# Performance work log

Measured on AMD Instinct MI355X. Metric: run time of the kernel, lower is better.

The kernel has to match this reference:

```python
import jax, jax.numpy as jnp
import numpy as np

B, TQ, M, D, H, F, L = 4, 512, 512, 1024, 16, 4096, 6
S = D // H
R = TQ + M  # relative-attention length = memory + query
CUTOFFS = [20000, 40000, 200000]
PROJ_FACTOR = 4
LN_EPS = 1e-6
NEG_INF = -1e9


def setup_inputs() -> dict:
    key = jax.random.key(0)
    ks = iter(jax.random.split(key, 64))

    def w(shape, scale=0.02):
        return jax.random.normal(next(ks), shape, jnp.float32) * scale

    inp = {}
    inp['token_ids'] = jax.random.randint(next(ks), (B, TQ), 0, CUTOFFS[-1])
    inp['memories'] = w((L, B, M, D))
    starts = [0] + CUTOFFS
    pf = 1
    for i in range(len(CUTOFFS)):
        psize = max(1, D // pf)
        inp['emb_table%d' % i] = w((starts[i + 1] - starts[i], psize))
        inp['emb_proj%d' % i] = w((psize, D))
        pf *= PROJ_FACTOR
    inp['wq'] = w((L, D, H, S)); inp['wk'] = w((L, D, H, S))
    inp['wv'] = w((L, D, H, S)); inp['wr'] = w((L, D, H, S))
    inp['wo'] = w((L, H, S, D))
    inp['content_bias'] = w((L, H, S)); inp['position_bias'] = w((L, H, S))
    inp['ln1_scale'] = jnp.ones((L, D)); inp['ln1_bias'] = jnp.zeros((L, D))
    inp['ln2_scale'] = jnp.ones((L, D)); inp['ln2_bias'] = jnp.zeros((L, D))
    inp['ffn_w1'] = w((L, D, F)); inp['ffn_b1'] = jnp.zeros((L, F))
    inp['ffn_w2'] = w((L, F, D)); inp['ffn_b2'] = jnp.zeros((L, D))
    return inp


def layernorm(x, scale, bias):
    mu = jnp.mean(x, axis=-1, keepdims=True)
    var = jnp.var(x, axis=-1, keepdims=True)
    return (x - mu) * jax.lax.rsqrt(var + LN_EPS) * scale + bias


def rel_shift(x):
    # x: [B, H, Q, R] -> shifted so position j aligns with relative distance
    b, h, q, r = x.shape
    x = jnp.pad(x, ((0, 0), (0, 0), (0, 0), (1, 0)))
    x = x.reshape(b, h, r + 1, q)[:, :, 1:, :]
    return x.reshape(b, h, q, r)


def positional_encoding(r_len, d):
    pos = jnp.arange(r_len - 1, -1, -1, dtype=jnp.float32)  # r_len-1 ... 0
    inv_freq = 1.0 / (10000.0 ** (jnp.arange(0, d, 2, dtype=jnp.float32) / d))
    sinusoid = pos[:, None] * inv_freq[None, :]
    return jnp.concatenate([jnp.sin(sinusoid), jnp.cos(sinusoid)], axis=-1)


def adaptive_embed(ids, tables, projs):
    # jit-friendly version of AdaptiveEmbedding.compute_embeddings:
    # gather per-cluster, project up to D, combine via masks.
    d = projs[0].shape[-1]
    y = jnp.zeros(ids.shape + (d,), jnp.float32)
    starts = [0] + CUTOFFS
    for tab, proj, lo, hi in zip(tables, projs, starts[:-1], starts[1:]):
        mask = (ids >= lo) & (ids < hi)
        idx = jnp.clip(ids - lo, 0, tab.shape[0] - 1)
        emb = jnp.einsum('btp,pd->btd', tab[idx], proj)
        y = y + jnp.where(mask[..., None], emb, 0.0)
    return y * (d ** 0.5)


def transformer_xl(token_ids, memories, emb_tables, emb_projs, wq, wk, wv, wr,
                   wo, content_bias, position_bias, ln1_scale, ln1_bias,
                   ln2_scale, ln2_bias, ffn_w1, ffn_b1, ffn_w2, ffn_b2):
    x = adaptive_embed(token_ids, emb_tables, emb_projs)  # [B, TQ, D]
    pe = positional_encoding(R, D)                        # [R, D]
    q_idx = jnp.arange(TQ)[:, None]
    r_idx = jnp.arange(R)[None, :]
    future = r_idx > q_idx + M                            # [TQ, R], True=masked
    scale = 1.0 / np.sqrt(S).astype(np.float32)
    for l in range(L):
        q = jnp.einsum('btd,dhs->bths', x, wq[l])
        kv_in = jnp.concatenate([memories[l], x], axis=1)  # [B, R, D]
        k = jnp.einsum('brd,dhs->brhs', kv_in, wk[l])
        v = jnp.einsum('brd,dhs->brhs', kv_in, wv[l])
        r = jnp.einsum('rd,dhs->rhs', pe, wr[l])
        ac = jnp.einsum('bqhs,brhs->bhqr', q + content_bias[l], k)
        bd = rel_shift(jnp.einsum('bqhs,rhs->bhqr', q + position_bias[l], r))
        scores = (ac + bd) * scale
        scores = jnp.where(future[None, None], NEG_INF, scores)
        attn = jax.nn.softmax(scores, axis=-1)
        ctx = jnp.einsum('bhqr,brhs->bqhs', attn, v)
        out = jnp.einsum('bqhs,hsd->bqd', ctx, wo[l])
        x = layernorm(x + out, ln1_scale[l], ln1_bias[l])
        h = jax.nn.relu(jnp.einsum('btd,df->btf', x, ffn_w1[l]) + ffn_b1[l])
        h = jnp.einsum('btf,fd->btd', h, ffn_w2[l]) + ffn_b2[l]
        x = layernorm(x + h, ln2_scale[l], ln2_bias[l])
    return x


def reference(token_ids, memories, emb_table0, emb_proj0, emb_table1,
              emb_proj1, emb_table2, emb_proj2, wq, wk, wv, wr, wo,
              content_bias, position_bias, ln1_scale, ln1_bias, ln2_scale,
              ln2_bias, ffn_w1, ffn_b1, ffn_w2, ffn_b2):
    return transformer_xl(
        token_ids, memories,
        [emb_table0, emb_table1, emb_table2],
        [emb_proj0, emb_proj1, emb_proj2],
        wq, wk, wv, wr, wo, content_bias, position_bias,
        ln1_scale, ln1_bias, ln2_scale, ln2_bias,
        ffn_w1, ffn_b1, ffn_w2, ffn_b2)
```

## Files before the change

kernel.cpp:

```cpp
#include <hip/hip_runtime.h>


#define Bc 4
#define TQc 512
#define Mc 512
#define Dc 1024
#define Hc 16
#define Sc 64
#define Fc 4096
#define Lc 6
#define Rc 1024
#define KCAT 1344
#define DDc ((size_t)Dc * Dc)
#define NEG_INF_F (-1e9f)

typedef unsigned short ushortT;
typedef __attribute__((ext_vector_type(8))) short bfrag;
typedef __attribute__((ext_vector_type(4))) float facc;

__device__ inline ushortT f2bf(float f) {
    unsigned int u = __builtin_bit_cast(unsigned int, f);
    u = (u + 0x7FFFu + ((u >> 16) & 1u)) >> 16;
    return (ushortT)u;
}

#define CP16(gp, lp)                                                        \
    __builtin_amdgcn_global_load_lds(                                       \
        (const __attribute__((address_space(1))) unsigned int*)(gp),        \
        (__attribute__((address_space(3))) unsigned int*)(lp), 16, 0, 0)

__device__ inline bfrag lds_frag(const ushortT* lds, int row, int cg) {
    int c = cg ^ (row & 7);
    return *reinterpret_cast<const bfrag*>(
        reinterpret_cast<const char*>(lds) + row * 128 + c * 16);
}

template<int BM, int BN, int OUTM, bool BIAS, bool RELU, bool DUALQ,
         bool KVSRC = false, bool KVOUT = false>
__global__ __launch_bounds__(256) void mgemm(
    const ushortT* __restrict__ A, const ushortT* __restrict__ A2,
    const ushortT* __restrict__ Bt,
    const float* __restrict__ bias, const float* __restrict__ bias2,
    float* __restrict__ Cf, ushortT* __restrict__ Cb, ushortT* __restrict__ Cb2,
    int K, int lda, int ldb, int ldc,
    long long sA1, long long sB1, long long sC1, float oscale) {
    constexpr int WTM = BM / 2, WTN = BN / 2;
    constexpr int FM = WTM / 16, FN = WTN / 16;
    __shared__ ushortT sA[2][BM * 64];
    __shared__ ushortT sB[2][BN * 64];
    int tid = threadIdx.x;
    int wave = tid >> 6, lane = tid & 63;
    int r16 = lane & 15, kgrp = lane >> 4;
    int wr = wave >> 1, wc = wave & 1;
    int z = blockIdx.z;
    A  += (long long)z * sA1;
    Bt += (long long)z * sB1;
    long long coff = (long long)z * sC1;
    if (OUTM != 1) Cf += coff;
    if (OUTM != 0 || DUALQ) Cb += coff;

    int row0 = blockIdx.y * BM, col0 = blockIdx.x * BN;
    facc acc[FM][FN] = {};

    auto STAGE = [&](int buf, int k0) {
        #pragma unroll
        for (int it = 0; it < BM / 32; ++it) {
            int s = it * 256 + tid;
            int row = s >> 3, c = s & 7;
            int cs = c ^ (row & 7);
            const char* g;
            if constexpr (KVSRC) {
                int arow = row0 + row;
                int bq = arow >> 10;
                int r = arow & 1023;
                if (r < Mc)
                    g = (const char*)(A + ((size_t)bq * Mc + r) * lda + k0) + cs * 16;
                else
                    g = (const char*)(A2 + ((size_t)bq * TQc + (r - Mc)) * lda + k0) + cs * 16;
            } else {
                g = (const char*)(A + (size_t)(row0 + row) * lda + k0) + cs * 16;
            }
            CP16(g, (char*)sA[buf] + s * 16);
        }
        #pragma unroll
        for (int it = 0; it < BN / 32; ++it) {
            int s = it * 256 + tid;
            int row = s >> 3, c = s & 7;
            int cs = c ^ (row & 7);
            CP16((const char*)(Bt + (size_t)(col0 + row) * ldb + k0) + cs * 16,
                 (char*)sB[buf] + s * 16);
        }
    };

    STAGE(0, 0);
    __syncthreads();
    int nk = K >> 6;
    for (int t = 0; t < nk; ++t) {
        int cur = t & 1;
        if (t + 1 < nk) STAGE(cur ^ 1, (t + 1) << 6);
        #pragma unroll
        for (int ks = 0; ks < 2; ++ks) {
            bfrag af[FM], bf[FN];
            #pragma unroll
            for (int mi = 0; mi < FM; ++mi)
                af[mi] = lds_frag(sA[cur], wr * WTM + mi * 16 + r16, ks * 4 + kgrp);
            #pragma unroll
            for (int ni = 0; ni < FN; ++ni)
                bf[ni] = lds_frag(sB[cur], wc * WTN + ni * 16 + r16, ks * 4 + kgrp);
            #pragma unroll
            for (int mi = 0; mi < FM; ++mi)
                #pragma unroll
                for (int ni = 0; ni < FN; ++ni)
                    acc[mi][ni] = __builtin_amdgcn_mfma_f32_16x16x32_bf16(
                        af[mi], bf[ni], acc[mi][ni], 0, 0, 0);
        }
        __syncthreads();
    }

    if constexpr (KVOUT) {
        if (col0 >= 1024) {
            ushortT* sT = (ushortT*)sA;
            int b = row0 >> 10, r0l = row0 & 1023;
            int h0 = (col0 - 1024) >> 6;
            #pragma unroll
            for (int p = 0; p < 2; ++p) {
                __syncthreads();
                if (wc == p) {
                    #pragma unroll
                    for (int mi = 0; mi < FM; ++mi)
                        #pragma unroll
                        for (int ni = 0; ni < FN; ++ni) {
                            int srow = ni * 16 + r16;
                            int cbase = wr * 64 + mi * 16 + kgrp * 4;
                            short4 s4;
                            s4.x = (short)f2bf(acc[mi][ni][0]);
                            s4.y = (short)f2bf(acc[mi][ni][1]);
                            s4.z = (short)f2bf(acc[mi][ni][2]);
                            s4.w = (short)f2bf(acc[mi][ni][3]);
                            *(short4*)(sT + srow * 132 + cbase) = s4;
                        }
                }
                __syncthreads();
                int h = h0 + p;
                #pragma unroll
                for (int it = 0; it < 4; ++it) {
                    int srow = it * 16 + (tid >> 4);
                    int rch = (tid & 15) * 8;
                    short4 lo = *(short4*)(sT + srow * 132 + rch);
                    short4 hi = *(short4*)(sT + srow * 132 + rch + 4);
                    ushortT* dst = Cb2 + ((size_t)((b * 16 + h) * 64 + srow)) * Rc
                                   + r0l + rch;
                    *(short4*)dst = lo;
                    *(short4*)(dst + 4) = hi;
                }
            }
            return;
        }
    }

    #pragma unroll
    for (int mi = 0; mi < FM; ++mi) {
        #pragma unroll
        for (int ni = 0; ni < FN; ++ni) {
            int gcol = col0 + wc * WTN + ni * 16 + r16;
            float bv = 0.0f, bv2 = 0.0f;
            if (BIAS || DUALQ) bv = bias[gcol];
            if (DUALQ) bv2 = bias2[gcol];
            #pragma unroll
            for (int j = 0; j < 4; ++j) {
                int grow = row0 + wr * WTM + mi * 16 + kgrp * 4 + j;
                float v = acc[mi][ni][j];
                if constexpr (DUALQ) {
                    Cb [(size_t)grow * ldc + gcol] = f2bf((v + bv) * oscale);
                    Cb2[(size_t)grow * ldc + gcol] = f2bf((v + bv2) * oscale);
                } else if constexpr (OUTM == 2) {
                    v *= oscale;
                    Cf[(size_t)grow * ldc + gcol] = v;
                    Cb[(size_t)grow * ldc + gcol] = f2bf(v);
                } else {
                    if (BIAS) v += bv;
                    if (RELU) v = fmaxf(v, 0.0f);
                    if constexpr (OUTM == 0)
                        Cf[(size_t)grow * ldc + gcol] = v;
                    else
                        Cb[(size_t)grow * ldc + gcol] = f2bf(v);
                }
            }
        }
    }
}

__global__ __launch_bounds__(256) void fused_attn(
    const ushortT* __restrict__ qc, const ushortT* __restrict__ qp,
    const ushortT* __restrict__ kb, const ushortT* __restrict__ vT,
    const ushortT* __restrict__ rp, ushortT* __restrict__ ctx) {
    int n_id = (int)(blockIdx.y << 3) | (int)blockIdx.x;
    int b0 = n_id & 1, b7 = (n_id >> 7) & 1, b8 = (n_id >> 8) & 1;
    int u = (b7 << 1) | b0;
    int qt = (b0 ^ b8) ? (7 - u) : u;
    int bh = (n_id >> 1) & 63;
    int b = bh >> 4, h = bh & 15;
    int q0 = qt * 64;
    __shared__ ushortT sQc[64 * 64], sQp[64 * 64];
    __shared__ ushortT sK[64 * 64], sV[64 * 64], sP[64 * 64];
    __shared__ ushortT sR[128 * 64];
    __shared__ float sBD[64 * 65];
    int tid = threadIdx.x;
    int lane = tid & 63, wq = tid >> 6;
    int r16 = lane & 15, kgrp = lane >> 4;

    const ushortT* qcb = qc + (size_t)(b * TQc + q0) * Dc + h * 64;
    const ushortT* qpb = qp + (size_t)(b * TQc + q0) * Dc + h * 64;
    const ushortT* kbb = kb + (size_t)b * Rc * 1024 + h * 64;
    const ushortT* vTb = vT + (size_t)bh * 64 * Rc;
    const ushortT* rpb = rp + h * 64;
    int rrbase0 = 448 - q0;

    #pragma unroll
    for (int it = 0; it < 2; ++it) {
        int s = it * 256 + tid;
        int row = s >> 3, c = s & 7;
        int cs = c ^ (row & 7);
        CP16((const char*)(qcb + (size_t)row * Dc) + cs * 16, (char*)sQc + s * 16);
        CP16((const char*)(qpb + (size_t)row * Dc) + cs * 16, (char*)sQp + s * 16);
        CP16((const char*)(kbb + (size_t)row * 1024) + cs * 16, (char*)sK + s * 16);
        CP16((const char*)(vTb + (size_t)row * Rc) + cs * 16, (char*)sV + s * 16);
    }
    #pragma unroll
    for (int hR = 0; hR < 2; ++hR) {
        #pragma unroll
        for (int it = 0; it < 2; ++it) {
            int s = it * 256 + tid;
            int row = s >> 3, c = s & 7;
            int cs = c ^ (row & 7);
            int gr = rrbase0 + hR * 64 + row;
            gr = gr > 1023 ? 1023 : gr;
            CP16((const char*)(rpb + (size_t)gr * Dc) + cs * 16,
                 (char*)sR + (hR * 64 + row) * 128 + cs * 16);
        }
    }

    facc accO[4] = {};
    float m[4] = {-1e30f, -1e30f, -1e30f, -1e30f};
    float lsum[4] = {};

    int iters = qt + 9;
    for (int itj = 0; itj < iters; ++itj) {
        int j0 = itj * 64;
        __syncthreads();

        facc aac[4] = {};
        facc abd[5] = {};
        __builtin_amdgcn_s_setprio(1);
        #pragma unroll
        for (int ks = 0; ks < 2; ++ks) {
            bfrag aq = lds_frag(sQc, wq * 16 + r16, ks * 4 + kgrp);
            bfrag ap = lds_frag(sQp, wq * 16 + r16, ks * 4 + kgrp);
            #pragma unroll
            for (int n = 0; n < 4; ++n) {
                bfrag bk = lds_frag(sK, n * 16 + r16, ks * 4 + kgrp);
                aac[n] = __builtin_amdgcn_mfma_f32_16x16x32_bf16(aq, bk, aac[n], 0, 0, 0);
            }
            #pragma unroll
            for (int n = 0; n < 5; ++n) {
                int t = 3 - wq + n;
                int ph = (itj ^ (t >> 2)) & 1;
                bfrag br = lds_frag(sR, ph * 64 + (t & 3) * 16 + r16, ks * 4 + kgrp);
                abd[n] = __builtin_amdgcn_mfma_f32_16x16x32_bf16(ap, br, abd[n], 0, 0, 0);
            }
        }
        __builtin_amdgcn_s_setprio(0);
        #pragma unroll
        for (int n = 0; n < 5; ++n) {
            int rl = (3 - wq + n) * 16 + r16;
            #pragma unroll
            for (int jj = 0; jj < 4; ++jj) {
                int ql = wq * 16 + kgrp * 4 + jj;
                int jl = rl + ql - 63;
                if (jl >= 0 && jl < 64) sBD[ql * 65 + jl] = abd[n][jj];
            }
        }

        bool lastit = (itj == iters - 1);
        float P[4][4];
        #pragma unroll
        for (int jj = 0; jj < 4; ++jj) {
            int ql = wq * 16 + kgrp * 4 + jj;
            float sv[4];
            #pragma unroll
            for (int n = 0; n < 4; ++n) {
                int jl = n * 16 + r16;
                sv[n] = aac[n][jj] + sBD[ql * 65 + jl];
            }
            if (lastit) {
                int qg = q0 + ql;
                #pragma unroll
                for (int n = 0; n < 4; ++n) {
                    int jg = j0 + n * 16 + r16;
                    if (jg > qg + Mc) sv[n] = NEG_INF_F;
                }
            }
            float mx = fmaxf(fmaxf(sv[0], sv[1]), fmaxf(sv[2], sv[3]));
            mx = fmaxf(mx, __shfl_xor(mx, 1));
            mx = fmaxf(mx, __shfl_xor(mx, 2));
            mx = fmaxf(mx, __shfl_xor(mx, 4));
            mx = fmaxf(mx, __shfl_xor(mx, 8));
            float mnew = fmaxf(m[jj], mx);
            float corr = __expf(m[jj] - mnew);
            m[jj] = mnew;
            float rs = 0.0f;
            #pragma unroll
            for (int n = 0; n < 4; ++n) {
                float p = __expf(sv[n] - mnew);
                P[n][jj] = p;
                rs += p;
            }
            rs += __shfl_xor(rs, 1);
            rs += __shfl_xor(rs, 2);
            rs += __shfl_xor(rs, 4);
            rs += __shfl_xor(rs, 8);
            lsum[jj] = lsum[jj] * corr + rs;
            #pragma unroll
            for (int n = 0; n < 4; ++n) accO[n][jj] *= corr;
        }
        #pragma unroll
        for (int jj = 0; jj < 4; ++jj) {
            int row = wq * 16 + kgrp * 4 + jj;
            #pragma unroll
            for (int n = 0; n < 4; ++n) {
                int col = n * 16 + r16;
                int boff = row * 128 + (((col >> 3) ^ (row & 7)) * 16) + (col & 7) * 2;
                *(ushortT*)((char*)sP + boff) = f2bf(P[n][jj]);
            }
        }
        __builtin_amdgcn_s_setprio(1);
        #pragma unroll
        for (int ks = 0; ks < 2; ++ks) {
            bfrag pa = lds_frag(sP, wq * 16 + r16, ks * 4 + kgrp);
            #pragma unroll
            for (int n = 0; n < 4; ++n) {
                bfrag bv = lds_frag(sV, n * 16 + r16, ks * 4 + kgrp);
                accO[n] = __builtin_amdgcn_mfma_f32_16x16x32_bf16(pa, bv, accO[n], 0, 0, 0);
            }
        }
        __builtin_amdgcn_s_setprio(0);
        __syncthreads();

        if (itj + 1 < iters) {
            int jn = j0 + 64;
            #pragma unroll
            for (int it2 = 0; it2 < 2; ++it2) {
                int s = it2 * 256 + tid;
                int row = s >> 3, c = s & 7;
                int cs = c ^ (row & 7);
                CP16((const char*)(kbb + (size_t)(jn + row) * 1024) + cs * 16,
                     (char*)sK + s * 16);
                CP16((const char*)(vTb + (size_t)row * Rc + jn) + cs * 16,
                     (char*)sV + s * 16);
            }
            int ph = itj & 1;
            int grb = jn - q0 + 512;
            #pragma unroll
            for (int it2 = 0; it2 < 2; ++it2) {
                int s = it2 * 256 + tid;
                int row = s >> 3, c = s & 7;
                int cs = c ^ (row & 7);
                int gr = grb + row;
                gr = gr > 1023 ? 1023 : gr;
                CP16((const char*)(rpb + (size_t)gr * Dc) + cs * 16,
                     (char*)sR + (ph * 64 + row) * 128 + cs * 16);
            }
        }
    }
    #pragma unroll
    for (int jj = 0; jj < 4; ++jj) {
        int qg = q0 + wq * 16 + kgrp * 4 + jj;
        float inv = 1.0f / lsum[jj];
        #pragma unroll
        for (int n = 0; n < 4; ++n) {
            int col = n * 16 + r16;
            ctx[(size_t)(b * TQc + qg) * Dc + h * 64 + col] = f2bf(accO[n][jj] * inv);
        }
    }
}

__global__ __launch_bounds__(256) void tr_f32_bf16(
    const float* __restrict__ in, ushortT* __restrict__ out, int R0, int C0,
    int ldout, int coff, long long inZ, long long outZ) {
    in += (long long)blockIdx.z * inZ;
    out += (long long)blockIdx.z * outZ;
    __shared__ float t[32][33];
    int tx = threadIdx.x & 31, ty = threadIdx.x >> 5;
    int c0 = blockIdx.x * 32, r0 = blockIdx.y * 32;
    #pragma unroll
    for (int i = 0; i < 4; ++i)
        t[ty + i * 8][tx] = in[(size_t)(r0 + ty + i * 8) * C0 + c0 + tx];
    __syncthreads();
    int c = threadIdx.x >> 3, rq = (threadIdx.x & 7) << 2;
    short4 s4;
    s4.x = (short)f2bf(t[rq + 0][c]);
    s4.y = (short)f2bf(t[rq + 1][c]);
    s4.z = (short)f2bf(t[rq + 2][c]);
    s4.w = (short)f2bf(t[rq + 3][c]);
    *(short4*)(out + (size_t)(c0 + c) * ldout + coff + r0 + rq) = s4;
}

__global__ __launch_bounds__(256) void tr_dxd5(
    const float* __restrict__ wr, const float* __restrict__ wq,
    const float* __restrict__ wk, const float* __restrict__ wv,
    const float* __restrict__ wo,
    ushortT* __restrict__ wrT, ushortT* __restrict__ wqT,
    ushortT* __restrict__ wkvT, ushortT* __restrict__ woT) {
    int sel = blockIdx.z / Lc, l = blockIdx.z % Lc;
    const float* in; ushortT* out;
    if (sel == 0)      { in = wr + l * DDc; out = wrT + l * DDc; }
    else if (sel == 1) { in = wq + l * DDc; out = wqT + l * DDc; }
    else if (sel == 2) { in = wk + l * DDc; out = wkvT + l * 2 * DDc; }
    else if (sel == 3) { in = wv + l * DDc; out = wkvT + l * 2 * DDc + DDc; }
    else               { in = wo + l * DDc; out = woT + l * DDc; }
    __shared__ float t[32][33];
    int tx = threadIdx.x & 31, ty = threadIdx.x >> 5;
    int c0 = blockIdx.x * 32, r0 = blockIdx.y * 32;
    #pragma unroll
    for (int i = 0; i < 4; ++i)
        t[ty + i * 8][tx] = in[(size_t)(r0 + ty + i * 8) * Dc + c0 + tx];
    __syncthreads();
    int c = threadIdx.x >> 3, rq = (threadIdx.x & 7) << 2;
    short4 s4;
    s4.x = (short)f2bf(t[rq + 0][c]);
    s4.y = (short)f2bf(t[rq + 1][c]);
    s4.z = (short)f2bf(t[rq + 2][c]);
    s4.w = (short)f2bf(t[rq + 3][c]);
    *(short4*)(out + (size_t)(c0 + c) * Dc + r0 + rq) = s4;
}

__global__ __launch_bounds__(256) void pos_enc_kernel(ushortT* __restrict__ pe) {
    int idx = blockIdx.x * 256 + threadIdx.x;
    int r = idx >> 10;
    int d = idx & 1023;
    float pos = (float)(Rc - 1 - r);
    int i = (d < 512) ? d : (d - 512);
    float inv_freq = 1.0f / powf(10000.0f, (2.0f * (float)i) / 1024.0f);
    float arg = pos * inv_freq;
    pe[idx] = f2bf((d < 512) ? sinf(arg) : cosf(arg));
}

__global__ __launch_bounds__(256) void gather_embed(
    const int* __restrict__ ids,
    const float* __restrict__ t0, const float* __restrict__ t1,
    const float* __restrict__ t2, ushortT* __restrict__ gcat) {
    int token = blockIdx.x;
    int id = ids[token];
    ushortT* row = gcat + (size_t)token * KCAT;
    short4 z4 = {0, 0, 0, 0};
    for (int t = threadIdx.x; t < KCAT / 4; t += 256)
        reinterpret_cast<short4*>(row)[t] = z4;
    __syncthreads();
    const float* tab; int psize, lo, o;
    if (id < 20000)      { tab = t0; psize = 1024; lo = 0;     o = 0; }
    else if (id < 40000) { tab = t1; psize = 256;  lo = 20000; o = 1024; }
    else                 { tab = t2; psize = 64;   lo = 40000; o = 1280; }
    const float* src = tab + (size_t)(id - lo) * psize;
    for (int p4 = threadIdx.x; p4 < psize / 4; p4 += 256) {
        float4 v = reinterpret_cast<const float4*>(src)[p4];
        short4 s4;
        s4.x = (short)f2bf(v.x); s4.y = (short)f2bf(v.y);
        s4.z = (short)f2bf(v.z); s4.w = (short)f2bf(v.w);
        reinterpret_cast<short4*>(row + o)[p4] = s4;
    }
}

__global__ __launch_bounds__(256) void cast_f32_bf16(
    const float* __restrict__ in, ushortT* __restrict__ o) {
    size_t i8 = ((size_t)blockIdx.x * 256 + threadIdx.x) * 8;
    const float4* m4 = (const float4*)(in + i8);
    float4 a = m4[0], c = m4[1];
    int4 p;
    p.x = (int)f2bf(a.x) | ((int)f2bf(a.y) << 16);
    p.y = (int)f2bf(a.z) | ((int)f2bf(a.w) << 16);
    p.z = (int)f2bf(c.x) | ((int)f2bf(c.y) << 16);
    p.w = (int)f2bf(c.z) | ((int)f2bf(c.w) << 16);
    *(int4*)(o + i8) = p;
}

template<int NP, bool CBIAS>
__global__ __launch_bounds__(256) void add_ln_kernel(
    const float* __restrict__ xin, const float* __restrict__ r0,
    const float* __restrict__ r1, const float* __restrict__ r2,
    const float* __restrict__ r3, const float* __restrict__ cbias,
    const float* __restrict__ scale, const float* __restrict__ bias,
    float* __restrict__ dst, ushortT* __restrict__ dstb) {
    int row = blockIdx.x * 4 + (threadIdx.x >> 6);
    int lane = threadIdx.x & 63;
    const float4* xr = (const float4*)(xin + (size_t)row * Dc);
    const float4* p0 = (const float4*)(r0 + (size_t)row * Dc);
    const float4* p1 = nullptr; const float4* p2 = nullptr; const float4* p3 = nullptr;
    if constexpr (NP > 1) p1 = (const float4*)(r1 + (size_t)row * Dc);
    if constexpr (NP > 2) p2 = (const float4*)(r2 + (size_t)row * Dc);
    if constexpr (NP > 3) p3 = (const float4*)(r3 + (size_t)row * Dc);
    const float4* cb4 = CBIAS ? (const float4*)cbias : nullptr;
    float4 v[4];
    float s = 0.0f, s2 = 0.0f;
    #pragma unroll
    for (int rep = 0; rep < 4; ++rep) {
        int idx = rep * 64 + lane;
        float4 a = xr[idx];
        float4 b = p0[idx];
        a.x += b.x; a.y += b.y; a.z += b.z; a.w += b.w;
        if constexpr (NP > 1) {
            float4 c1 = p1[idx];
            a.x += c1.x; a.y += c1.y; a.z += c1.z; a.w += c1.w;
        }
        if constexpr (NP > 2) {
            float4 c2 = p2[idx];
            a.x += c2.x; a.y += c2.y; a.z += c2.z; a.w += c2.w;
        }
        if constexpr (NP > 3) {
            float4 c3 = p3[idx];
            a.x += c3.x; a.y += c3.y; a.z += c3.z; a.w += c3.w;
        }
        if constexpr (CBIAS) {
            float4 cbv = cb4[idx];
            a.x += cbv.x; a.y += cbv.y; a.z += cbv.z; a.w += cbv.w;
        }
        v[rep] = a;
        s += a.x + a.y + a.z + a.w;
        s2 += a.x * a.x + a.y * a.y + a.z * a.z + a.w * a.w;
    }
    #pragma unroll
    for (int o = 1; o < 64; o <<= 1) {
        s += __shfl_xor(s, o);
        s2 += __shfl_xor(s2, o);
    }
    float mean = s * (1.0f / Dc);
    float var = s2 * (1.0f / Dc) - mean * mean;
    float rstd = rsqrtf(var + 1e-6f);
    float4* d4 = (float4*)(dst + (size_t)row * Dc);
    short4* db4 = (short4*)(dstb + (size_t)row * Dc);
    const float4* sc4 = (const float4*)scale;
    const float4* bi4 = (const float4*)bias;
    #pragma unroll
    for (int rep = 0; rep < 4; ++rep) {
        int idx = rep * 64 + lane;
        float4 scv = sc4[idx], biv = bi4[idx];
        float4 a = v[rep];
        float4 o;
        o.x = (a.x - mean) * rstd * scv.x + biv.x;
        o.y = (a.y - mean) * rstd * scv.y + biv.y;
        o.z = (a.z - mean) * rstd * scv.z + biv.z;
        o.w = (a.w - mean) * rstd * scv.w + biv.w;
        d4[idx] = o;
        short4 ob;
        ob.x = (short)f2bf(o.x); ob.y = (short)f2bf(o.y);
        ob.z = (short)f2bf(o.z); ob.w = (short)f2bf(o.w);
        db4[idx] = ob;
    }
}

extern "C" void kernel_launch(void* const* d_in, const int* in_sizes, int n_in,
                              void* d_out, int out_size, void* d_ws, size_t ws_size,
                              hipStream_t stream) {
    const int*   token_ids = (const int*)d_in[0];
    const float* memories  = (const float*)d_in[1];
    const float* tab0 = (const float*)d_in[2];
    const float* prj0 = (const float*)d_in[3];
    const float* tab1 = (const float*)d_in[4];
    const float* prj1 = (const float*)d_in[5];
    const float* tab2 = (const float*)d_in[6];
    const float* prj2 = (const float*)d_in[7];
    const float* wq = (const float*)d_in[8];
    const float* wk = (const float*)d_in[9];
    const float* wv = (const float*)d_in[10];
    const float* wr = (const float*)d_in[11];
    const float* wo = (const float*)d_in[12];
    const float* cb = (const float*)d_in[13];
    const float* pb = (const float*)d_in[14];
    const float* ln1s = (const float*)d_in[15];
    const float* ln1b = (const float*)d_in[16];
    const float* ln2s = (const float*)d_in[17];
    const float* ln2b = (const float*)d_in[18];
    const float* w1 = (const float*)d_in[19];
    const float* b1 = (const float*)d_in[20];
    const float* w2 = (const float*)d_in[21];
    const float* b2 = (const float*)d_in[22];
    float* out = (float*)d_out;

    char* wsb = (char*)d_ws;
    size_t off = 0;
    auto alloc = [&](size_t bytes) {
        char* p = wsb + off;
        off += (bytes + 255) & ~(size_t)255;
        return p;
    };
    const size_t DD = DDc;
    const size_t TD = (size_t)Bc * TQc * Dc;
    const size_t DF = (size_t)Dc * Fc;
    ushortT* pe_b  = (ushortT*)alloc((size_t)Rc * Dc * 2);
    ushortT* wrT   = (ushortT*)alloc((size_t)Lc * DD * 2);
    ushortT* rpA   = (ushortT*)alloc((size_t)Lc * Rc * Dc * 2);
    ushortT* wqT   = (ushortT*)alloc((size_t)Lc * DD * 2);
    ushortT* wkvT  = (ushortT*)alloc((size_t)Lc * 2 * DD * 2);
    ushortT* woT   = (ushortT*)alloc((size_t)Lc * DD * 2);
    ushortT* w1T   = (ushortT*)alloc((size_t)Lc * DF * 2);
    ushortT* w2T   = (ushortT*)alloc((size_t)Lc * DF * 2);
    ushortT* memb  = (ushortT*)alloc((size_t)Lc * Bc * Mc * Dc * 2);
    ushortT* gcat  = (ushortT*)alloc((size_t)Bc * TQc * KCAT * 2);
    ushortT* WcatT = (ushortT*)alloc((size_t)Dc * KCAT * 2);
    float*   x     = (float*)alloc(TD * 4);
    ushortT* xb    = (ushortT*)alloc(TD * 2);
    ushortT* qc    = (ushortT*)alloc(TD * 2);
    ushortT* qp    = (ushortT*)alloc(TD * 2);
    ushortT* kbuf  = (ushortT*)alloc((size_t)Bc * Rc * 1024 * 2);
    ushortT* vT    = (ushortT*)alloc((size_t)Bc * Rc * Dc * 2);
    ushortT* ctxb  = (ushortT*)alloc(TD * 2);
    float*   obp   = (float*)alloc(4 * TD * 4);
    ushortT* hb    = (ushortT*)alloc((size_t)Bc * TQc * Fc * 2);

    pos_enc_kernel<<<(Rc * Dc) / 256, 256, 0, stream>>>(pe_b);
    gather_embed<<<Bc * TQc, 256, 0, stream>>>(token_ids, tab0, tab1, tab2, gcat);
    tr_f32_bf16<<<dim3(32, 32), 256, 0, stream>>>(prj0, WcatT, 1024, 1024, KCAT, 0, 0, 0);
    tr_f32_bf16<<<dim3(32, 8), 256, 0, stream>>>(prj1, WcatT, 256, 1024, KCAT, 1024, 0, 0);
    tr_f32_bf16<<<dim3(32, 2), 256, 0, stream>>>(prj2, WcatT, 64, 1024, KCAT, 1280, 0, 0);
    mgemm<64, 64, 2, false, false, false><<<dim3(16, 32), 256, 0, stream>>>(
        gcat, nullptr, WcatT, nullptr, nullptr, x, xb, nullptr,
        KCAT, KCAT, KCAT, Dc, 0, 0, 0, 32.0f);

    tr_dxd5<<<dim3(32, 32, 5 * Lc), 256, 0, stream>>>(
        wr, wq, wk, wv, wo, wrT, wqT, wkvT, woT);
    tr_f32_bf16<<<dim3(128, 32, Lc), 256, 0, stream>>>(w1, w1T, Dc, Fc, Dc, 0, DF, DF);
    tr_f32_bf16<<<dim3(32, 128, Lc), 256, 0, stream>>>(w2, w2T, Fc, Dc, Fc, 0, DF, DF);
    cast_f32_bf16<<<(Lc * Bc * Mc * Dc) / (256 * 8), 256, 0, stream>>>(memories, memb);
    mgemm<64, 64, 1, false, false, false><<<dim3(16, 16, Lc), 256, 0, stream>>>(
        pe_b, nullptr, wrT, nullptr, nullptr, nullptr, rpA, nullptr,
        Dc, Dc, Dc, Dc, 0, (long long)DD, (long long)Rc * Dc, 1.0f);

    for (int l = 0; l < Lc; ++l) {
        const ushortT* membl = memb + (size_t)l * Bc * Mc * Dc;
        mgemm<64, 64, 1, false, false, true><<<dim3(16, 32), 256, 0, stream>>>(
            xb, nullptr, wqT + (size_t)l * DD, cb + (size_t)l * Dc, pb + (size_t)l * Dc,
            nullptr, qc, qp, Dc, Dc, Dc, Dc, 0, 0, 0, 0.125f);
        mgemm<128, 128, 1, false, false, false, true, true>
            <<<dim3(16, 32), 256, 0, stream>>>(
            membl, xb, wkvT + (size_t)l * 2 * DD, nullptr, nullptr,
            nullptr, kbuf, vT, Dc, Dc, Dc, 1024, 0, 0, 0, 1.0f);

        fused_attn<<<dim3(8, 64), 256, 0, stream>>>(
            qc, qp, kbuf, vT, rpA + (size_t)l * Rc * Dc, ctxb);

        mgemm<64, 64, 0, false, false, false><<<dim3(16, 32), 256, 0, stream>>>(
            ctxb, nullptr, woT + (size_t)l * DD, nullptr, nullptr, obp, nullptr, nullptr,
            Dc, Dc, Dc, Dc, 0, 0, 0, 1.0f);
        add_ln_kernel<1, false><<<Bc * TQc / 4, 256, 0, stream>>>(
            x, obp, nullptr, nullptr, nullptr, nullptr,
            ln1s + (size_t)l * Dc, ln1b + (size_t)l * Dc, x, xb);
        mgemm<128, 128, 1, true, true, false><<<dim3(32, 16), 256, 0, stream>>>(
            xb, nullptr, w1T + (size_t)l * DF, b1 + (size_t)l * Fc, nullptr,
            nullptr, hb, nullptr, Dc, Dc, Dc, Fc, 0, 0, 0, 1.0f);
        mgemm<128, 128, 0, false, false, false><<<dim3(8, 16, 4), 256, 0, stream>>>(
            hb, nullptr, w2T + (size_t)l * DF, nullptr, nullptr, obp, nullptr, nullptr,
            1024, Fc, Fc, Dc, 1024, 1024, (long long)TD, 1.0f);
        add_ln_kernel<4, true><<<Bc * TQc / 4, 256, 0, stream>>>(
            x, obp, obp + TD, obp + 2 * TD, obp + 3 * TD, b2 + (size_t)l * Dc,
            ln2s + (size_t)l * Dc, ln2b + (size_t)l * Dc,
            (l == Lc - 1) ? out : x, xb);
    }
}
```

Baseline: 1.256 ms.

## Double-buffer K/V and triple-buffer R tiles in fused attention, hoist Q fragments

The fused relative attention kernel now prefetches the next K/V tile into a second buffer and the R tile two steps ahead into a three-slot ring, issued at the start of each iteration so the copies overlap compute. This removes the trailing barrier and the serialized load phase. Q fragments are loaded into registers once, and the BD scratch is XOR-swizzled and aliased over the Q buffers. P now uses a per-wave slice of that region. The cost is a larger shared-memory footprint (72KB), which may lower occupancy, plus more complex buffer indexing with aliasing hazards between the BD and P regions.

```diff
diff --git a/kernel.cpp b/kernel.cpp
--- a/kernel.cpp
+++ b/kernel.cpp
@@ -201,13 +201,17 @@
     int bh = (n_id >> 1) & 63;
     int b = bh >> 4, h = bh & 15;
     int q0 = qt * 64;
-    __shared__ ushortT sQc[64 * 64], sQp[64 * 64];
-    __shared__ ushortT sK[64 * 64], sV[64 * 64], sP[64 * 64];
-    __shared__ ushortT sR[128 * 64];
-    __shared__ float sBD[64 * 65];
+    __shared__ __align__(16) char smem[73728];
+    ushortT* sQc = (ushortT*)smem;
+    ushortT* sQp = (ushortT*)(smem + 8192);
+    float*   sBD = (float*)smem;
+    ushortT* sK  = (ushortT*)(smem + 16384);
+    ushortT* sV  = (ushortT*)(smem + 32768);
+    ushortT* sR  = (ushortT*)(smem + 49152);
     int tid = threadIdx.x;
     int lane = tid & 63, wq = tid >> 6;
     int r16 = lane & 15, kgrp = lane >> 4;
+    char* sPb = smem + wq * 4096;
 
     const ushortT* qcb = qc + (size_t)(b * TQc + q0) * Dc + h * 64;
     const ushortT* qpb = qp + (size_t)(b * TQc + q0) * Dc + h * 64;
@@ -215,6 +219,7 @@
     const ushortT* vTb = vT + (size_t)bh * 64 * Rc;
     const ushortT* rpb = rp + h * 64;
     int rrbase0 = 448 - q0;
+    int iters = qt + 9;
 
     #pragma unroll
     for (int it = 0; it < 2; ++it) {
@@ -236,37 +241,73 @@
             int gr = rrbase0 + hR * 64 + row;
             gr = gr > 1023 ? 1023 : gr;
             CP16((const char*)(rpb + (size_t)gr * Dc) + cs * 16,
-                 (char*)sR + (hR * 64 + row) * 128 + cs * 16);
-        }
-    }
+                 (char*)sR + hR * 8192 + s * 16);
+        }
+    }
+    __syncthreads();
+
+    bfrag hqc[2], hqp[2];
+    #pragma unroll
+    for (int ks = 0; ks < 2; ++ks) {
+        hqc[ks] = lds_frag(sQc, wq * 16 + r16, ks * 4 + kgrp);
+        hqp[ks] = lds_frag(sQp, wq * 16 + r16, ks * 4 + kgrp);
+    }
+    __syncthreads();
 
     facc accO[4] = {};
     float m[4] = {-1e30f, -1e30f, -1e30f, -1e30f};
     float lsum[4] = {};
 
-    int iters = qt + 9;
     for (int itj = 0; itj < iters; ++itj) {
         int j0 = itj * 64;
         __syncthreads();
+        int cur = itj & 1;
+        int ph0 = itj % 3, ph1 = (itj + 1) % 3;
+
+        if (itj + 1 < iters) {
+            int jn = j0 + 64;
+            #pragma unroll
+            for (int it2 = 0; it2 < 2; ++it2) {
+                int s = it2 * 256 + tid;
+                int row = s >> 3, c = s & 7;
+                int cs = c ^ (row & 7);
+                CP16((const char*)(kbb + (size_t)(jn + row) * 1024) + cs * 16,
+                     (char*)sK + (cur ^ 1) * 8192 + s * 16);
+                CP16((const char*)(vTb + (size_t)row * Rc + jn) + cs * 16,
+                     (char*)sV + (cur ^ 1) * 8192 + s * 16);
+            }
+        }
+        if (itj + 2 <= iters) {
+            int L = itj + 2;
+            int p2 = L % 3;
+            #pragma unroll
+            for (int it2 = 0; it2 < 2; ++it2) {
+                int s = it2 * 256 + tid;
+                int row = s >> 3, c = s & 7;
+                int cs = c ^ (row & 7);
+                int gr = rrbase0 + L * 64 + row;
+                gr = gr > 1023 ? 1023 : gr;
+                CP16((const char*)(rpb + (size_t)gr * Dc) + cs * 16,
+                     (char*)sR + p2 * 8192 + s * 16);
+            }
+        }
 
         facc aac[4] = {};
         facc abd[5] = {};
         __builtin_amdgcn_s_setprio(1);
         #pragma unroll
         for (int ks = 0; ks < 2; ++ks) {
-            bfrag aq = lds_frag(sQc, wq * 16 + r16, ks * 4 + kgrp);
-            bfrag ap = lds_frag(sQp, wq * 16 + r16, ks * 4 + kgrp);
             #pragma unroll
             for (int n = 0; n < 4; ++n) {
-                bfrag bk = lds_frag(sK, n * 16 + r16, ks * 4 + kgrp);
-                aac[n] = __builtin_amdgcn_mfma_f32_16x16x32_bf16(aq, bk, aac[n], 0, 0, 0);
+                bfrag bk = lds_frag(sK + cur * 4096, n * 16 + r16, ks * 4 + kgrp);
+                aac[n] = __builtin_amdgcn_mfma_f32_16x16x32_bf16(hqc[ks], bk, aac[n], 0, 0, 0);
             }
             #pragma unroll
             for (int n = 0; n < 5; ++n) {
                 int t = 3 - wq + n;
-                int ph = (itj ^ (t >> 2)) & 1;
-                bfrag br = lds_frag(sR, ph * 64 + (t & 3) * 16 + r16, ks * 4 + kgrp);
-                abd[n] = __builtin_amdgcn_mfma_f32_16x16x32_bf16(ap, br, abd[n], 0, 0, 0);
+                int p = (t >> 2) ? ph1 : ph0;
+                bfrag br = lds_frag(sR + p * 4096, (t & 3) * 16 + r16, ks * 4 + kgrp);
+                abd[n] = __builtin_amdgcn_mfma_f32_16x16x32_bf16(hqp[ks], br, abd[n], 0, 0, 0);
             }
         }
         __builtin_amdgcn_s_setprio(0);
@@ -277,7 +318,8 @@
             for (int jj = 0; jj < 4; ++jj) {
                 int ql = wq * 16 + kgrp * 4 + jj;
                 int jl = rl + ql - 63;
-                if (jl >= 0 && jl < 64) sBD[ql * 65 + jl] = abd[n][jj];
+                if (jl >= 0 && jl < 64)
+                    sBD[ql * 64 + (jl ^ (((ql >> 2) & 1) << 4))] = abd[n][jj];
             }
         }
 
@@ -286,11 +328,12 @@
         #pragma unroll
         for (int jj = 0; jj < 4; ++jj) {
             int ql = wq * 16 + kgrp * 4 + jj;
+            int swz = ((ql >> 2) & 1) << 4;
             float sv[4];
             #pragma unroll
             for (int n = 0; n < 4; ++n) {
                 int jl = n * 16 + r16;
-                sv[n] = aac[n][jj] + sBD[ql * 65 + jl];
+                sv[n] = aac[n][jj] + sBD[ql * 64 + (jl ^ swz)];
             }
             if (lastit) {
                 int qg = q0 + ql;
@@ -329,48 +372,21 @@
             #pragma unroll
             for (int n = 0; n < 4; ++n) {
                 int col = n * 16 + r16;
-                int boff = row * 128 + (((col >> 3) ^ (row & 7)) * 16) + (col & 7) * 2;
-                *(ushortT*)((char*)sP + boff) = f2bf(P[n][jj]);
+                int boff = (row & 15) * 128 + (((col >> 3) ^ (row & 7)) * 16) + (col & 7) * 2;
+                *(ushortT*)(sPb + boff) = f2bf(P[n][jj]);
             }
         }
         __builtin_amdgcn_s_setprio(1);
         #pragma unroll
         for (int ks = 0; ks < 2; ++ks) {
-            bfrag pa = lds_frag(sP, wq * 16 + r16, ks * 4 + kgrp);
+            bfrag pa = *(const bfrag*)(sPb + r16 * 128 + (((ks * 4 + kgrp) ^ (r16 & 7)) * 16));
             #pragma unroll
             for (int n = 0; n < 4; ++n) {
-                bfrag bv = lds_frag(sV, n * 16 + r16, ks * 4 + kgrp);
+                bfrag bv = lds_frag(sV + cur * 4096, n * 16 + r16, ks * 4 + kgrp);
                 accO[n] = __builtin_amdgcn_mfma_f32_16x16x32_bf16(pa, bv, accO[n], 0, 0, 0);
             }
         }
         __builtin_amdgcn_s_setprio(0);
-        __syncthreads();
-
-        if (itj + 1 < iters) {
-            int jn = j0 + 64;
-            #pragma unroll
-            for (int it2 = 0; it2 < 2; ++it2) {
-                int s = it2 * 256 + tid;
-                int row = s >> 3, c = s & 7;
-                int cs = c ^ (row & 7);
-                CP16((const char*)(kbb + (size_t)(jn + row) * 1024) + cs * 16,
-                     (char*)sK + s * 16);
-                CP16((const char*)(vTb + (size_t)row * Rc + jn) + cs * 16,
-                     (char*)sV + s * 16);
-            }
-            int ph = itj & 1;
-            int grb = jn - q0 + 512;
-            #pragma unroll
-            for (int it2 = 0; it2 < 2; ++it2) {
-                int s = it2 * 256 + tid;
-                int row = s >> 3, c = s & 7;
-                int cs = c ^ (row & 7);
-                int gr = grb + row;
-                gr = gr > 1023 ? 1023 : gr;
-                CP16((const char*)(rpb + (size_t)gr * Dc) + cs * 16,
-                     (char*)sR + (ph * 64 + row) * 128 + cs * 16);
-            }
-        }
     }
     #pragma unroll
     for (int jj = 0; jj < 4; ++jj) {
```

Result: no change. 1.259 ms (+0.2%).
